# Optimization experiments

Hardware: AMD Instinct MI355X
Metric: run time of the kernel (lower is better)

Reference implementation:

```python
import jax, jax.numpy as jnp
import numpy as np

K = 16          # knn neighbors (init kwarg k)
GROUPS = 4      # GroupNorm groups
EPS = 1e-5
SLOPE = 0.2     # LeakyReLU negative slope


def fps(xyz, n):
    """Farthest point sampling. xyz: (B,N,3) -> idx (B,n). First index is 0 (pointnet2 convention)."""
    B, N, _ = xyz.shape

    def step(carry, _):
        dist, last = carry
        p = jnp.take_along_axis(xyz, last[:, None, None], axis=1)  # (B,1,3)
        d = jnp.sum((xyz - p) ** 2, axis=-1)                       # (B,N)
        dist = jnp.minimum(dist, d)
        nxt = jnp.argmax(dist, axis=-1).astype(jnp.int32)
        return (dist, nxt), nxt

    init = (jnp.full((B, N), jnp.inf, xyz.dtype), jnp.zeros((B,), jnp.int32))
    _, idxs = jax.lax.scan(step, init, None, length=n - 1)  # (n-1, B)
    return jnp.concatenate([jnp.zeros((B, 1), jnp.int32), idxs.T], axis=1)


def graph_feature(cq, fq, ck, fk):
    """DGCNN edge features. cq:(B,Q,3) fq:(B,Q,C) ck:(B,N,3) fk:(B,N,C) -> (B,Q,K,2C)."""
    d2 = (jnp.sum(cq * cq, -1)[:, :, None]
          - 2.0 * jnp.einsum('bqc,bnc->bqn', cq, ck)
          + jnp.sum(ck * ck, -1)[:, None, :])        # (B,Q,N)
    _, idx = jax.lax.top_k(-d2, K)                    # (B,Q,K) nearest first
    nb = jax.vmap(lambda f_, i_: f_[i_])(fk, idx)     # (B,Q,K,C)
    ctr = jnp.broadcast_to(fq[:, :, None, :], nb.shape)
    return jnp.concatenate([nb - ctr, ctr], axis=-1)


def conv_gn_lrelu(y, W, gw, gb):
    """1x1 Conv2d (no bias) + GroupNorm(4) + LeakyReLU(0.2). y: (B,Q,K,Cin), W: (Cout,Cin)."""
    y = jnp.einsum('bqkc,oc->bqko', y, W)
    B, Q, Kk, C = y.shape
    yg = y.reshape(B, Q * Kk, GROUPS, C // GROUPS)
    m = yg.mean(axis=(1, 3), keepdims=True)
    v = yg.var(axis=(1, 3), keepdims=True)
    y = ((yg - m) * jax.lax.rsqrt(v + EPS)).reshape(B, Q, Kk, C) * gw + gb
    return jnp.where(y > 0, y, SLOPE * y)


def setup_inputs() -> dict:
    key = jax.random.key(0)
    ks = jax.random.split(key, 16)
    B, N = 8, 4096
    s = lambda k_, shape, scale=0.1: (jax.random.normal(k_, shape, jnp.float32) * scale)
    return {
        'x': jax.random.normal(ks[0], (B, N, 7), jnp.float32),
        'W_in': s(ks[1], (8, 3), 0.5), 'b_in': s(ks[2], (8,), 0.02),
        'W1': s(ks[3], (32, 16), 0.2), 'g1w': jnp.ones((32,), jnp.float32), 'g1b': jnp.zeros((32,), jnp.float32),
        'W2': s(ks[4], (64, 64), 0.1), 'g2w': jnp.ones((64,), jnp.float32), 'g2b': jnp.zeros((64,), jnp.float32),
        'W3': s(ks[5], (64, 128), 0.1), 'g3w': jnp.ones((64,), jnp.float32), 'g3b': jnp.zeros((64,), jnp.float32),
        'W4': s(ks[6], (128, 128), 0.1), 'g4w': jnp.ones((128,), jnp.float32), 'g4b': jnp.zeros((128,), jnp.float32),
        'num0': 1024,
    }


def reference(x, W_in, b_in, W1, g1w, g1b, W2, g2w, g2b, W3, g3w, g3b, W4, g4w, g4b, num0):
    coor, normal, plane = x[..., :3], x[..., 3:6], x[..., 6:7]   # (B,N,3),(B,N,3),(B,N,1)

    # input_trans: Conv1d(3,8,1)
    f = jnp.einsum('bnc,oc->bno', coor, W_in) + b_in             # (B,N,8)

    g = graph_feature(coor, f, coor, f)                          # (B,N,K,16)
    f = conv_gn_lrelu(g, W1, g1w, g1b).max(axis=2)               # (B,N,32)

    idx = fps(coor, num0)
    gather = lambda a: jnp.take_along_axis(a, idx[:, :, None], axis=1)
    coor_q, normal_q, plane_q, f_q = gather(coor), gather(normal), gather(plane), gather(f)

    g = graph_feature(coor_q, f_q, coor, f)                      # (B,num0,K,64)
    f = conv_gn_lrelu(g, W2, g2w, g2b).max(axis=2)               # (B,num0,64)
    coor, normal, plane = coor_q, normal_q, plane_q

    g = graph_feature(coor, f, coor, f)                          # (B,num0,K,128)
    f = conv_gn_lrelu(g, W3, g3w, g3b).max(axis=2)               # (B,num0,64)

    idx = fps(coor, num0)  # source uses num[0] again
    gather = lambda a: jnp.take_along_axis(a, idx[:, :, None], axis=1)
    coor_q, normal_q, plane_q, f_q = gather(coor), gather(normal), gather(plane), gather(f)

    g = graph_feature(coor_q, f_q, coor, f)                      # (B,num0,K,128)
    f = conv_gn_lrelu(g, W4, g4w, g4b).max(axis=2)               # (B,num0,128)

    return coor_q, f, normal_q, plane_q
```

## Files before the change

kernel.cpp:

```cpp
#include <hip/hip_runtime.h>
#include <cstdint>

static constexpr int B   = 8;
static constexpr int N0  = 4096;
static constexpr int NQ  = 1024;
static constexpr int KNB = 16;

__device__ __forceinline__ unsigned long long wave_max_u64_l63(unsigned long long k) {
#define STEPU_(ctrl)                                                                    \
  {                                                                                     \
    unsigned lo_ = (unsigned)k, hi_ = (unsigned)(k >> 32);                              \
    unsigned plo_ = (unsigned)__builtin_amdgcn_update_dpp((int)lo_, (int)lo_, ctrl,     \
                                                          0xf, 0xf, false);             \
    unsigned phi_ = (unsigned)__builtin_amdgcn_update_dpp((int)hi_, (int)hi_, ctrl,     \
                                                          0xf, 0xf, false);             \
    unsigned long long pk_ = ((unsigned long long)phi_ << 32) | plo_;                   \
    if (pk_ > k) k = pk_;                                                               \
  }
  STEPU_(0x111) STEPU_(0x112) STEPU_(0x114) STEPU_(0x118) STEPU_(0x142) STEPU_(0x143)
#undef STEPU_
  return k;
}

__device__ __forceinline__ float gnf(float mx, float mn, float scv, float mo, float gb) {
  float sel = (scv >= 0.f) ? mx : mn;
  float v = (sel - mo) * scv + gb;
  return (v > 0.f) ? v : 0.2f * v;
}

__global__ void prep_kernel(const float* __restrict__ x,
                            const float* __restrict__ W_in,
                            const float* __restrict__ b_in,
                            const float* __restrict__ W1,
                            float4* __restrict__ c4, float* __restrict__ nrm,
                            float* __restrict__ pl, float* __restrict__ f0,
                            float* __restrict__ ctrY1) {
  int i = blockIdx.x * 256 + threadIdx.x;
  if (i >= B * N0) return;
  const float* xp = x + (size_t)i * 7;
  float cx = xp[0], cy = xp[1], cz = xp[2];
  float kk = __fadd_rn(__fadd_rn(__fmul_rn(cx, cx), __fmul_rn(cy, cy)), __fmul_rn(cz, cz));
  c4[i] = make_float4(cx, cy, cz, kk);
  nrm[i * 3 + 0] = xp[3]; nrm[i * 3 + 1] = xp[4]; nrm[i * 3 + 2] = xp[5];
  pl[i] = xp[6];
  float f[8];
#pragma unroll
  for (int o = 0; o < 8; o++) {
    f[o] = cx * W_in[o * 3 + 0] + cy * W_in[o * 3 + 1] + cz * W_in[o * 3 + 2] + b_in[o];
    f0[(size_t)i * 8 + o] = f[o];
  }
#pragma unroll
  for (int o = 0; o < 32; o++) {
    const float* wp = W1 + (size_t)o * 16 + 8;
    float acc = 0.f;
#pragma unroll
    for (int c = 0; c < 8; c++) acc = fmaf(f[c], wp[c], acc);
    ctrY1[(size_t)i * 32 + o] = acc;
  }
}

template <int NC>
__device__ __forceinline__ void knn_body(int bq, int lane,
                                         const float4* __restrict__ q4,
                                         const float4* __restrict__ k4,
                                         int Q, int Nk, int* __restrict__ out) {
  int b = bq / Q;
  float4 q = q4[bq];
  const float4* kb = k4 + (size_t)b * Nk + lane;
  const float INF    = __int_as_float(0x7f800000);
  const float NEGINF = __int_as_float(0xff800000);
  float myd = INF;
  int   myi = 0;
  float kth = INF;
  const bool isl0 = (lane & 15) == 0;
  constexpr int G = (NC >= 8) ? 8 : NC;
  for (int c0 = 0; c0 < NC; c0 += G) {
    float dg[G];
#pragma unroll
    for (int u = 0; u < G; u++) {
      float4 kp = kb[(c0 + u) * 64];
      float dot = __fadd_rn(__fadd_rn(__fmul_rn(q.x, kp.x), __fmul_rn(q.y, kp.y)),
                            __fmul_rn(q.z, kp.z));
      dg[u] = __fadd_rn(__fsub_rn(q.w, __fmul_rn(2.0f, dot)), kp.w);
    }
#pragma unroll
    for (int u = 0; u < G; u++) {
      float d = dg[u];
      unsigned long long msk = __ballot(d < kth);
      while (msk) {
        int j = __builtin_ctzll(msk);
        float dv = __int_as_float(__builtin_amdgcn_readlane(__float_as_int(d), j));
        int   iv = (c0 + u) * 64 + j;
        bool gt = (myd > dv);
        float pd = __int_as_float(__builtin_amdgcn_update_dpp(
            0, __float_as_int(myd), 0x111, 0xf, 0xf, true));
        int   pi = __builtin_amdgcn_update_dpp(0, myi, 0x111, 0xf, 0xf, true);
        pd = isl0 ? NEGINF : pd;
        bool tp = (pd > dv);
        float nd = tp ? pd : dv;
        int   ni = tp ? pi : iv;
        myd = gt ? nd : myd;
        myi = gt ? ni : myi;
        kth = __int_as_float(__builtin_amdgcn_readlane(__float_as_int(myd), 15));
        msk = __ballot(d < kth);
        msk = (j < 63) ? (msk & (~0ull << (j + 1))) : 0ull;
      }
    }
  }
  if (lane < KNB) out[(size_t)bq * KNB + lane] = myi;
}

template <int NPTS>
__device__ __forceinline__ void fps_body(const float4* __restrict__ cb, int* w) {
  constexpr int BLK = 256;
  constexpr int M = NPTS / BLK;
  constexpr int NW = BLK / 64;
  __shared__ __align__(16) float2 sxy[NPTS];
  __shared__ float szz[NPTS];
  __shared__ __align__(16) unsigned long long skey[2][NW];
  const int tid = threadIdx.x;
  const int wid = tid >> 6, lane = tid & 63;
  float cx[M], cy[M], cz[M], dist[M];
#pragma unroll
  for (int i = 0; i < M; i++) {
    float4 p = cb[tid * M + i];
    cx[i] = p.x; cy[i] = p.y; cz[i] = p.z;
    dist[i] = 3.4e38f;
    sxy[tid * M + i] = make_float2(p.x, p.y);
    szz[tid * M + i] = p.z;
  }
  w[0] = w[1] = w[2] = w[3] = 0;
  float4 p0 = cb[0];
  float px = p0.x, py = p0.y, pz = p0.z;
  __syncthreads();
  for (int t = 1; t < NQ; t++) {
    float bv = -1.f; int bi = 0;
#pragma unroll
    for (int i = 0; i < M; i++) {
      float dx = __fsub_rn(cx[i], px), dy = __fsub_rn(cy[i], py), dz = __fsub_rn(cz[i], pz);
      float d = __fadd_rn(__fadd_rn(__fmul_rn(dx, dx), __fmul_rn(dy, dy)), __fmul_rn(dz, dz));
      float dd = dist[i]; dd = (d < dd) ? d : dd; dist[i] = dd;
      if (dd > bv) { bv = dd; bi = tid * M + i; }
    }
    unsigned long long k =
        ((unsigned long long)__float_as_uint(bv) << 12) | (unsigned)(4095 - bi);
    k = wave_max_u64_l63(k);
    int p = t & 1;
    if (lane == 63) skey[p][wid] = k;
    __syncthreads();
    ulonglong2 ab = *(const ulonglong2*)&skey[p][0];
    ulonglong2 cd = *(const ulonglong2*)&skey[p][2];
    unsigned long long m0 = (ab.x > ab.y) ? ab.x : ab.y;
    unsigned long long m1 = (cd.x > cd.y) ? cd.x : cd.y;
    unsigned long long mk = (m0 > m1) ? m0 : m1;
    int win = 4095 - (int)(mk & 0xFFFull);
    float2 pxy = sxy[win];
    px = pxy.x; py = pxy.y; pz = szz[win];
    if (t == tid) w[0] = win;
    if (t == tid + 256) w[1] = win;
    if (t == tid + 512) w[2] = win;
    if (t == tid + 768) w[3] = win;
  }
}

template <int NC, int CF, int CO>
__device__ __forceinline__ void knnec_body(
    int blkid, const float4* __restrict__ q4, const float4* __restrict__ k4,
    const float* __restrict__ fq, const float* __restrict__ fk,
    const float* __restrict__ Wfull, const float* __restrict__ ctrY,
    const int* __restrict__ ridx,
    float* __restrict__ ymin, float* __restrict__ ymax,
    float* __restrict__ gstats, int Q, int Nk) {
  constexpr int J = CO / 4;
  constexpr int SEC = J * CF + 8;
  __shared__ float Wl[4 * SEC];
  __shared__ float sstat[8];
  for (int t = threadIdx.x; t < CO * CF; t += 256) {
    int o = t / CF, c = t % CF;
    Wl[(o / J) * SEC + (o % J) * CF + c] = Wfull[(size_t)o * (2 * CF) + c];
  }
  if (threadIdx.x < 8) sstat[threadIdx.x] = 0.0f;
  __syncthreads();
  const int wid = threadIdx.x >> 6, lane = threadIdx.x & 63;
  const int bq = blkid * 4 + wid;
  const int b = bq / Q;
  float4 q = q4[bq];
  const float4* kb = k4 + (size_t)b * Nk + lane;
  const float INF    = __int_as_float(0x7f800000);
  const float NEGINF = __int_as_float(0xff800000);
  float myd = INF;
  int   myi = 0;
  float kth = INF;
  const bool isl0 = (lane & 15) == 0;
  constexpr int G = (NC >= 8) ? 8 : NC;
  for (int c0 = 0; c0 < NC; c0 += G) {
    float dg[G];
#pragma unroll
    for (int u = 0; u < G; u++) {
      float4 kp = kb[(c0 + u) * 64];
      float dot = __fadd_rn(__fadd_rn(__fmul_rn(q.x, kp.x), __fmul_rn(q.y, kp.y)),
                            __fmul_rn(q.z, kp.z));
      dg[u] = __fadd_rn(__fsub_rn(q.w, __fmul_rn(2.0f, dot)), kp.w);
    }
#pragma unroll
    for (int u = 0; u < G; u++) {
      float d = dg[u];
      unsigned long long msk = __ballot(d < kth);
      while (msk) {
        int j = __builtin_ctzll(msk);
        float dv = __int_as_float(__builtin_amdgcn_readlane(__float_as_int(d), j));
        int   iv = (c0 + u) * 64 + j;
        bool gt = (myd > dv);
        float pd = __int_as_float(__builtin_amdgcn_update_dpp(
            0, __float_as_int(myd), 0x111, 0xf, 0xf, true));
        int   pi = __builtin_amdgcn_update_dpp(0, myi, 0x111, 0xf, 0xf, true);
        pd = isl0 ? NEGINF : pd;
        bool tp = (pd > dv);
        float nd = tp ? pd : dv;
        int   nI = tp ? pi : iv;
        myd = gt ? nd : myd;
        myi = gt ? nI : myi;
        kth = __int_as_float(__builtin_amdgcn_readlane(__float_as_int(myd), 15));
        msk = __ballot(d < kth);
        msk = (j < 63) ? (msk & (~0ull << (j + 1))) : 0ull;
      }
    }
  }
  const int g = lane >> 4;
  const int ni = myi;
  const float* nbp = fk + (size_t)(b * Nk + ni) * CF;
  const float* cp = ridx ? fq + ((size_t)b * Nk + ridx[bq]) * CF
                         : fq + (size_t)bq * CF;
  float acc[J];
#pragma unroll
  for (int j = 0; j < J; j++) acc[j] = 0.0f;
  const float* wg = &Wl[g * SEC];
#pragma unroll
  for (int c = 0; c < CF; c += 4) {
    float4 nb4 = *(const float4*)(nbp + c);
    float4 c4  = *(const float4*)(cp + c);
    float e0 = nb4.x - c4.x, e1 = nb4.y - c4.y, e2 = nb4.z - c4.z, e3 = nb4.w - c4.w;
#pragma unroll
    for (int j = 0; j < J; j++) {
      float4 w4 = *(const float4*)(wg + j * CF + c);
      acc[j] = fmaf(e0, w4.x, acc[j]);
      acc[j] = fmaf(e1, w4.y, acc[j]);
      acc[j] = fmaf(e2, w4.z, acc[j]);
      acc[j] = fmaf(e3, w4.w, acc[j]);
    }
  }
  float s = 0.f, s2 = 0.f;
  const float* cyp = ctrY + (size_t)bq * CO + g * J;
#pragma unroll
  for (int j = 0; j < J; j++) {
    float y = acc[j] + cyp[j];
    acc[j] = y;
    s += y; s2 = fmaf(y, y, s2);
  }
  float mn[J];
#pragma unroll
  for (int j = 0; j < J; j++) mn[j] = acc[j];
#pragma unroll
  for (int m = 1; m < 16; m <<= 1) {
#pragma unroll
    for (int j = 0; j < J; j++) {
      float a = __shfl_xor(acc[j], m); if (a > acc[j]) acc[j] = a;
      float c2 = __shfl_xor(mn[j], m); if (c2 < mn[j]) mn[j] = c2;
    }
    s  += __shfl_xor(s, m);
    s2 += __shfl_xor(s2, m);
  }
  if ((lane & 15) == 0) {
    float* mnp = ymin + (size_t)bq * CO + g * J;
    float* mxp = ymax + (size_t)bq * CO + g * J;
#pragma unroll
    for (int j = 0; j < J; j++) { mnp[j] = mn[j]; mxp[j] = acc[j]; }
    atomicAdd(&sstat[g], s);
    atomicAdd(&sstat[4 + g], s2);
  }
  __syncthreads();
  if (threadIdx.x < 8) atomicAdd(&gstats[b * 8 + threadIdx.x], sstat[threadIdx.x]);
}

template <int NC, int CF, int CO, bool HAS_KNN>
__device__ __forceinline__ void ec_gn_core(
    int blkid, const float4* __restrict__ q4, const float4* __restrict__ k4,
    const int* __restrict__ knn,
    const float* __restrict__ yminP, const float* __restrict__ ymaxP,
    const float* __restrict__ gstP, const float* __restrict__ gwP,
    const float* __restrict__ gbP, float invP,
    const float* __restrict__ Wfull, const int* __restrict__ ridx,
    float* __restrict__ ymin, float* __restrict__ ymax,
    float* __restrict__ gstats, int Q, int Nk) {
  constexpr int J = CO / 4;
  constexpr int SEC = J * CF + 8;
  __shared__ float Wl[4 * SEC];
  __shared__ float sstat[8];
  __shared__ __align__(16) float t_scv[CF];
  __shared__ __align__(16) float t_mo[CF];
  __shared__ __align__(16) float t_gb[CF];
  __shared__ __align__(16) float wfc[4][CF];
  __shared__ float scy[4][CO];
  const int b = (blkid * 4) / Q;
  for (int t = threadIdx.x; t < CO * CF; t += 256) {
    int o = t / CF, c = t % CF;
    Wl[(o / J) * SEC + (o % J) * CF + c] = Wfull[(size_t)o * (2 * CF) + c];
  }
  if (threadIdx.x < CF) {
    int c = threadIdx.x;
    int gg = c / (CF / 4);
    float m  = gstP[b * 8 + gg] * invP;
    float s2 = gstP[b * 8 + 4 + gg] * invP;
    float rs = rsqrtf(s2 - m * m + 1e-5f);
    t_scv[c] = gwP[c] * rs;
    t_mo[c]  = m;
    t_gb[c]  = gbP[c];
  }
  if (threadIdx.x < 8) sstat[threadIdx.x] = 0.0f;
  __syncthreads();
  const int wid = threadIdx.x >> 6, lane = threadIdx.x & 63;
  const int bq = blkid * 4 + wid;
  size_t cbase = (ridx ? ((size_t)b * Nk + ridx[bq]) : (size_t)bq) * CF;
  if (lane < CF)
    wfc[wid][lane] = gnf(ymaxP[cbase + lane], yminP[cbase + lane],
                         t_scv[lane], t_mo[lane], t_gb[lane]);
  for (int oo = lane; oo < CO; oo += 64) {
    const float* wp = Wfull + (size_t)oo * (2 * CF) + CF;
    float acc0 = 0.f;
#pragma unroll
    for (int c = 0; c < CF; c++) acc0 = fmaf(wfc[wid][c], wp[c], acc0);
    scy[wid][oo] = acc0;
  }
  int ni;
  if (HAS_KNN) {
    float4 q = q4[bq];
    const float4* kb = k4 + (size_t)b * Nk + lane;
    const float INF    = __int_as_float(0x7f800000);
    const float NEGINF = __int_as_float(0xff800000);
    float myd = INF;
    int   myi = 0;
    float kth = INF;
    const bool isl0 = (lane & 15) == 0;
    constexpr int G = (NC >= 8) ? 8 : NC;
    for (int c0 = 0; c0 < NC; c0 += G) {
      float dg[G];
#pragma unroll
      for (int u = 0; u < G; u++) {
        float4 kp = kb[(c0 + u) * 64];
        float dot = __fadd_rn(__fadd_rn(__fmul_rn(q.x, kp.x), __fmul_rn(q.y, kp.y)),
                              __fmul_rn(q.z, kp.z));
        dg[u] = __fadd_rn(__fsub_rn(q.w, __fmul_rn(2.0f, dot)), kp.w);
      }
#pragma unroll
      for (int u = 0; u < G; u++) {
        float d = dg[u];
        unsigned long long msk = __ballot(d < kth);
        while (msk) {
          int j = __builtin_ctzll(msk);
          float dv = __int_as_float(__builtin_amdgcn_readlane(__float_as_int(d), j));
          int   iv = (c0 + u) * 64 + j;
          bool gt = (myd > dv);
          float pd = __int_as_float(__builtin_amdgcn_update_dpp(
              0, __float_as_int(myd), 0x111, 0xf, 0xf, true));
          int   pi = __builtin_amdgcn_update_dpp(0, myi, 0x111, 0xf, 0xf, true);
          pd = isl0 ? NEGINF : pd;
          bool tp = (pd > dv);
          float nd = tp ? pd : dv;
          int   nI = tp ? pi : iv;
          myd = gt ? nd : myd;
          myi = gt ? nI : myi;
          kth = __int_as_float(__builtin_amdgcn_readlane(__float_as_int(myd), 15));
          msk = __ballot(d < kth);
          msk = (j < 63) ? (msk & (~0ull << (j + 1))) : 0ull;
        }
      }
    }
    ni = myi;
  } else {
    ni = knn[(size_t)bq * KNB + (lane & 15)];
  }
  const int g = lane >> 4;
  size_t nbase = ((size_t)b * Nk + ni) * CF;
  float acc[J];
#pragma unroll
  for (int j = 0; j < J; j++) acc[j] = 0.0f;
  const float* wg = &Wl[g * SEC];
#pragma unroll
  for (int c = 0; c < CF; c += 4) {
    float4 mx4 = *(const float4*)(ymaxP + nbase + c);
    float4 mn4 = *(const float4*)(yminP + nbase + c);
    float4 sc4 = *(const float4*)(&t_scv[c]);
    float4 mo4 = *(const float4*)(&t_mo[c]);
    float4 gb4 = *(const float4*)(&t_gb[c]);
    float4 c4  = *(const float4*)(&wfc[wid][c]);
    float e0 = gnf(mx4.x, mn4.x, sc4.x, mo4.x, gb4.x) - c4.x;
    float e1 = gnf(mx4.y, mn4.y, sc4.y, mo4.y, gb4.y) - c4.y;
    float e2 = gnf(mx4.z, mn4.z, sc4.z, mo4.z, gb4.z) - c4.z;
    float e3 = gnf(mx4.w, mn4.w, sc4.w, mo4.w, gb4.w) - c4.w;
#pragma unroll
    for (int j = 0; j < J; j++) {
      float4 w4 = *(const float4*)(wg + j * CF + c);
      acc[j] = fmaf(e0, w4.x, acc[j]);
      acc[j] = fmaf(e1, w4.y, acc[j]);
      acc[j] = fmaf(e2, w4.z, acc[j]);
      acc[j] = fmaf(e3, w4.w, acc[j]);
    }
  }
  float s = 0.f, s2 = 0.f;
#pragma unroll
  for (int j = 0; j < J; j++) {
    float y = acc[j] + scy[wid][g * J + j];
    acc[j] = y;
    s += y; s2 = fmaf(y, y, s2);
  }
  float mn[J];
#pragma unroll
  for (int j = 0; j < J; j++) mn[j] = acc[j];
#pragma unroll
  for (int m = 1; m < 16; m <<= 1) {
#pragma unroll
    for (int j = 0; j < J; j++) {
      float a = __shfl_xor(acc[j], m); if (a > acc[j]) acc[j] = a;
      float c2 = __shfl_xor(mn[j], m); if (c2 < mn[j]) mn[j] = c2;
    }
    s  += __shfl_xor(s, m);
    s2 += __shfl_xor(s2, m);
  }
  if ((lane & 15) == 0) {
    float* mnp = ymin + (size_t)bq * CO + g * J;
    float* mxp = ymax + (size_t)bq * CO + g * J;
#pragma unroll
    for (int j = 0; j < J; j++) { mnp[j] = mn[j]; mxp[j] = acc[j]; }
    atomicAdd(&sstat[g], s);
    atomicAdd(&sstat[4 + g], s2);
  }
  __syncthreads();
  if (threadIdx.x < 8) atomicAdd(&gstats[b * 8 + threadIdx.x], sstat[threadIdx.x]);
}

__global__ __launch_bounds__(256, 2) void mega1_kernel(
    const float4* __restrict__ c40, const float* __restrict__ nrm,
    const float* __restrict__ pl, const float* __restrict__ f0,
    const float* __restrict__ W1, const float* __restrict__ ctrY1,
    int* __restrict__ idx1,
    float4* __restrict__ c4q1, float* __restrict__ nq1, float* __restrict__ pq1,
    float* __restrict__ ymin, float* __restrict__ ymax, float* __restrict__ gst1) {
  int blk = blockIdx.x;
  if (blk < 8) {
    const int b = blk, tid = threadIdx.x;
    const float4* cb = c40 + (size_t)b * N0;
    int w[4];
    fps_body<N0>(cb, w);
    int* idxb = idx1 + (size_t)b * NQ;
#pragma unroll
    for (int u = 0; u < 4; u++) {
      int r = tid + u * 256;
      int s = (u == 0 && tid == 0) ? 0 : w[u];
      idxb[r] = s;
      c4q1[(size_t)b * NQ + r] = cb[s];
      const float* np = nrm + ((size_t)b * N0 + s) * 3;
      float* ndp = nq1 + ((size_t)b * NQ + r) * 3;
      ndp[0] = np[0]; ndp[1] = np[1]; ndp[2] = np[2];
      pq1[(size_t)b * NQ + r] = pl[(size_t)b * N0 + s];
    }
  } else {
    knnec_body<64, 8, 32>(blk - 8, c40, c40, f0, f0, W1, ctrY1, nullptr,
                          ymin, ymax, gst1, N0, N0);
  }
}

__global__ __launch_bounds__(256, 2) void mega2_kernel(
    const float4* __restrict__ c40, const float4* __restrict__ c4q1,
    const float* __restrict__ nq1, const float* __restrict__ pq1,
    const float* __restrict__ yminA, const float* __restrict__ ymaxA,
    const float* __restrict__ gst1, const float* __restrict__ g1w,
    const float* __restrict__ g1b, float inv1,
    const int* __restrict__ idx1, const float* __restrict__ W2,
    float* __restrict__ yminB, float* __restrict__ ymaxB, float* __restrict__ gst2,
    int* __restrict__ idx2, float4* __restrict__ c4q2,
    float* __restrict__ cq2out, float* __restrict__ nq2out,
    float* __restrict__ pq2out, int* __restrict__ knnB) {
  int blk = blockIdx.x;
  if (blk < 8) {
    const int b = blk, tid = threadIdx.x;
    const float4* cqb = c4q1 + (size_t)b * NQ;
    int w[4];
    fps_body<NQ>(cqb, w);
    int* idxb = idx2 + (size_t)b * NQ;
#pragma unroll
    for (int u = 0; u < 4; u++) {
      int r = tid + u * 256;
      int s = (u == 0 && tid == 0) ? 0 : w[u];
      idxb[r] = s;
      float4 c = cqb[s];
      c4q2[(size_t)b * NQ + r] = c;
      float* cd = cq2out + ((size_t)b * NQ + r) * 3;
      cd[0] = c.x; cd[1] = c.y; cd[2] = c.z;
      const float* np = nq1 + ((size_t)b * NQ + s) * 3;
      float* ndp = nq2out + ((size_t)b * NQ + r) * 3;
      ndp[0] = np[0]; ndp[1] = np[1]; ndp[2] = np[2];
      pq2out[(size_t)b * NQ + r] = pq1[(size_t)b * NQ + s];
    }
  } else if (blk < 8 + 2048) {
    ec_gn_core<64, 32, 64, true>(blk - 8, c4q1, c40, nullptr,
                                 yminA, ymaxA, gst1, g1w, g1b, inv1,
                                 W2, idx1, yminB, ymaxB, gst2, NQ, N0);
  } else {
    int bq = (blk - (8 + 2048)) * 4 + (threadIdx.x >> 6);
    knn_body<16>(bq, threadIdx.x & 63, c4q1, c4q1, NQ, NQ, knnB);
  }
}

__global__ __launch_bounds__(256) void ec3g_kernel(
    const int* __restrict__ knnB,
    const float* __restrict__ yminB, const float* __restrict__ ymaxB,
    const float* __restrict__ gst2, const float* __restrict__ g2w,
    const float* __restrict__ g2b, float inv2,
    const float* __restrict__ W3,
    float* __restrict__ yminC, float* __restrict__ ymaxC, float* __restrict__ gst3) {
  ec_gn_core<16, 64, 64, false>(blockIdx.x, nullptr, nullptr, knnB,
                                yminB, ymaxB, gst2, g2w, g2b, inv2,
                                W3, nullptr, yminC, ymaxC, gst3, NQ, NQ);
}

__global__ __launch_bounds__(256) void mega3g_kernel(
    const float4* __restrict__ c4q1, const float4* __restrict__ c4q2,
    const float* __restrict__ yminC, const float* __restrict__ ymaxC,
    const float* __restrict__ gst3, const float* __restrict__ g3w,
    const float* __restrict__ g3b, float inv3,
    const int* __restrict__ idx2, const float* __restrict__ W4,
    float* __restrict__ yminD, float* __restrict__ ymaxD, float* __restrict__ gst4) {
  ec_gn_core<16, 64, 128, true>(blockIdx.x, c4q2, c4q1, nullptr,
                                yminC, ymaxC, gst3, g3w, g3b, inv3,
                                W4, idx2, yminD, ymaxD, gst4, NQ, NQ);
}

template <int CO>
__global__ void gn_out_kernel(const float* __restrict__ ymin, const float* __restrict__ ymax,
                              const float* __restrict__ gstats, const float* __restrict__ gw,
                              const float* __restrict__ gb, float* __restrict__ fout,
                              int total, int Q, float inv_cnt) {
  int i = blockIdx.x * 256 + threadIdx.x;
  if (i >= total) return;
  constexpr int J = CO / 4;
  int o = i % CO; int bq = i / CO; int b = bq / Q;
  int g = o / J;
  float m  = gstats[b * 8 + g] * inv_cnt;
  float s2 = gstats[b * 8 + 4 + g] * inv_cnt;
  float rs = rsqrtf(s2 - m * m + 1e-5f);
  float sc = gw[o] * rs;
  float sel = (sc >= 0.f) ? ymax[i] : ymin[i];
  float v = (sel - m) * sc + gb[o];
  fout[i] = (v > 0.f) ? v : 0.2f * v;
}

extern "C" void kernel_launch(void* const* d_in, const int* in_sizes, int n_in,
                              void* d_out, int out_size, void* d_ws, size_t ws_size,
                              hipStream_t stream) {
  (void)in_sizes; (void)n_in; (void)out_size; (void)ws_size;
  const float* x    = (const float*)d_in[0];
  const float* W_in = (const float*)d_in[1];
  const float* b_in = (const float*)d_in[2];
  const float* W1   = (const float*)d_in[3];
  const float* g1w  = (const float*)d_in[4];
  const float* g1b  = (const float*)d_in[5];
  const float* W2   = (const float*)d_in[6];
  const float* g2w  = (const float*)d_in[7];
  const float* g2b  = (const float*)d_in[8];
  const float* W3   = (const float*)d_in[9];
  const float* g3w  = (const float*)d_in[10];
  const float* g3b  = (const float*)d_in[11];
  const float* W4   = (const float*)d_in[12];
  const float* g4w  = (const float*)d_in[13];
  const float* g4b  = (const float*)d_in[14];

  float* ws = (float*)d_ws;
  size_t o_c40   = 0;
  size_t o_nrm   = o_c40   + (size_t)B * N0 * 4;
  size_t o_pl    = o_nrm   + (size_t)B * N0 * 3;
  size_t o_f0    = o_pl    + (size_t)B * N0;
  size_t o_ctrY1 = o_f0    + (size_t)B * N0 * 8;
  size_t o_yAmin = o_ctrY1 + (size_t)B * N0 * 32;
  size_t o_yAmax = o_yAmin + (size_t)B * N0 * 32;
  size_t o_yBmin = o_yAmax + (size_t)B * N0 * 32;
  size_t o_yBmax = o_yBmin + (size_t)B * NQ * 64;
  size_t o_yCmin = o_yBmax + (size_t)B * NQ * 64;
  size_t o_yCmax = o_yCmin + (size_t)B * NQ * 64;
  size_t o_knnB  = o_yCmax + (size_t)B * NQ * 64;
  size_t o_gst   = o_knnB  + (size_t)B * NQ * KNB;
  size_t o_idx1  = o_gst   + 4 * B * 8;
  size_t o_idx2  = o_idx1  + (size_t)B * NQ;
  size_t o_c4q1  = o_idx2  + (size_t)B * NQ;
  size_t o_c4q2  = o_c4q1  + (size_t)B * NQ * 4;
  size_t o_nq1   = o_c4q2  + (size_t)B * NQ * 4;
  size_t o_pq1   = o_nq1   + (size_t)B * NQ * 3;

  float4* c40   = (float4*)(ws + o_c40);
  float*  nrm   = ws + o_nrm;    float* pl    = ws + o_pl;
  float*  f0    = ws + o_f0;     float* ctrY1 = ws + o_ctrY1;
  float*  yAmin = ws + o_yAmin;  float* yAmax = ws + o_yAmax;
  float*  yBmin = ws + o_yBmin;  float* yBmax = ws + o_yBmax;
  float*  yCmin = ws + o_yCmin;  float* yCmax = ws + o_yCmax;
  float*  yDmin = ctrY1;
  float*  yDmax = yAmin;
  int*    knnB  = (int*)(ws + o_knnB);
  float*  gst   = ws + o_gst;
  int*    idx1  = (int*)(ws + o_idx1);
  int*    idx2  = (int*)(ws + o_idx2);
  float4* c4q1  = (float4*)(ws + o_c4q1);
  float4* c4q2  = (float4*)(ws + o_c4q2);
  float*  nq1   = ws + o_nq1;    float* pq1   = ws + o_pq1;

  float* out  = (float*)d_out;
  float* cq2  = out;
  float* fout = out + (size_t)B * NQ * 3;
  float* nq2  = fout + (size_t)B * NQ * 128;
  float* pq2  = nq2 + (size_t)B * NQ * 3;

  const float inv1 = 1.0f / (4096.0f * 16.0f * 8.0f);
  const float inv2 = 1.0f / (1024.0f * 16.0f * 16.0f);
  const float inv3 = 1.0f / (1024.0f * 16.0f * 16.0f);
  const float inv4 = 1.0f / (1024.0f * 16.0f * 32.0f);

  hipMemsetAsync(gst, 0, 4 * B * 8 * sizeof(float), stream);

  prep_kernel<<<(B * N0 + 255) / 256, 256, 0, stream>>>(x, W_in, b_in, W1,
                                                        c40, nrm, pl, f0, ctrY1);

  mega1_kernel<<<8 + 8192, 256, 0, stream>>>(c40, nrm, pl, f0, W1, ctrY1,
                                             idx1, c4q1, nq1, pq1,
                                             yAmin, yAmax, gst + 0);

  mega2_kernel<<<8 + 2048 + 2048, 256, 0, stream>>>(
      c40, c4q1, nq1, pq1, yAmin, yAmax, gst + 0, g1w, g1b, inv1,
      idx1, W2, yBmin, yBmax, gst + B * 8,
      idx2, c4q2, cq2, nq2, pq2, knnB);

  ec3g_kernel<<<B * NQ / 4, 256, 0, stream>>>(
      knnB, yBmin, yBmax, gst + B * 8, g2w, g2b, inv2, W3,
      yCmin, yCmax, gst + 2 * B * 8);

  mega3g_kernel<<<B * NQ / 4, 256, 0, stream>>>(
      c4q1, c4q2, yCmin, yCmax, gst + 2 * B * 8, g3w, g3b, inv3,
      idx2, W4, yDmin, yDmax, gst + 3 * B * 8);

  gn_out_kernel<128><<<(B * NQ * 128 + 255) / 256, 256, 0, stream>>>(
      yDmin, yDmax, gst + 3 * B * 8, g4w, g4b, fout, B * NQ * 128, NQ, inv4);
}
```

Baseline: 1.438 ms.

## Run second-stage FPS in a single wavefront with barrier-free DPP reductions

Replaces the 256-thread farthest-point-sampling loop over the 1024 sampled points with a single-wavefront version. Each lane keeps 16 points in registers, and the argmax uses DPP shuffles plus ballot/readlane instead of LDS exchanges and a __syncthreads per iteration. This targets the per-step barrier and cross-wave latency on the serial FPS chain in mega2. Launch bounds are relaxed from 2 to 1 blocks per CU, which may raise register use and lower occupancy for the edge-conv and kNN blocks that share the kernel.

```diff
diff --git a/kernel.cpp b/kernel.cpp
--- a/kernel.cpp
+++ b/kernel.cpp
@@ -160,6 +160,50 @@
     if (t == tid + 256) w[1] = win;
     if (t == tid + 512) w[2] = win;
     if (t == tid + 768) w[3] = win;
+  }
+}
+
+template <int NPTS>
+__device__ __forceinline__ void fps1w_body(const float4* __restrict__ cb,
+                                           int* __restrict__ swin) {
+  constexpr int M = NPTS / 64;
+  const int lane = threadIdx.x;
+  float cx[M], cy[M], cz[M], dist[M];
+#pragma unroll
+  for (int i = 0; i < M; i++) {
+    float4 p = cb[lane * M + i];
+    cx[i] = p.x; cy[i] = p.y; cz[i] = p.z;
+    dist[i] = 3.4e38f;
+  }
+  float4 p0 = cb[0];
+  float px = p0.x, py = p0.y, pz = p0.z;
+  for (int t = 1; t < NQ; t++) {
+    float bv = -1.f; int bi = 0;
+    float bx = px, by = py, bz = pz;
+#pragma unroll
+    for (int i = 0; i < M; i++) {
+      float dx = __fsub_rn(cx[i], px), dy = __fsub_rn(cy[i], py), dz = __fsub_rn(cz[i], pz);
+      float d = __fadd_rn(__fadd_rn(__fmul_rn(dx, dx), __fmul_rn(dy, dy)), __fmul_rn(dz, dz));
+      float dd = dist[i]; dd = (d < dd) ? d : dd; dist[i] = dd;
+      if (dd > bv) { bv = dd; bi = lane * M + i; bx = cx[i]; by = cy[i]; bz = cz[i]; }
+    }
+    float wm = bv;
+#define SMAX_(ctrl)                                                                     \
+  {                                                                                     \
+    int t_ = __builtin_amdgcn_update_dpp(__float_as_int(wm), __float_as_int(wm), ctrl,  \
+                                         0xf, 0xf, false);                              \
+    wm = fmaxf(wm, __int_as_float(t_));                                                 \
+  }
+    SMAX_(0x111) SMAX_(0x112) SMAX_(0x114) SMAX_(0x118) SMAX_(0x142) SMAX_(0x143)
+#undef SMAX_
+    float wmax = __int_as_float(__builtin_amdgcn_readlane(__float_as_int(wm), 63));
+    unsigned long long tied = __ballot(bv == wmax);
+    int L = (int)__builtin_ctzll(tied);
+    int win = __builtin_amdgcn_readlane(bi, L);
+    px = __int_as_float(__builtin_amdgcn_readlane(__float_as_int(bx), L));
+    py = __int_as_float(__builtin_amdgcn_readlane(__float_as_int(by), L));
+    pz = __int_as_float(__builtin_amdgcn_readlane(__float_as_int(bz), L));
+    if (lane == 0) swin[t] = win;
   }
 }
 
@@ -469,7 +513,7 @@
   }
 }
 
-__global__ __launch_bounds__(256, 2) void mega2_kernel(
+__global__ __launch_bounds__(256, 1) void mega2_kernel(
     const float4* __restrict__ c40, const float4* __restrict__ c4q1,
     const float* __restrict__ nq1, const float* __restrict__ pq1,
     const float* __restrict__ yminA, const float* __restrict__ ymaxA,
@@ -482,24 +526,26 @@
     float* __restrict__ pq2out, int* __restrict__ knnB) {
   int blk = blockIdx.x;
   if (blk < 8) {
-    const int b = blk, tid = threadIdx.x;
-    const float4* cqb = c4q1 + (size_t)b * NQ;
-    int w[4];
-    fps_body<NQ>(cqb, w);
-    int* idxb = idx2 + (size_t)b * NQ;
-#pragma unroll
-    for (int u = 0; u < 4; u++) {
-      int r = tid + u * 256;
-      int s = (u == 0 && tid == 0) ? 0 : w[u];
-      idxb[r] = s;
-      float4 c = cqb[s];
-      c4q2[(size_t)b * NQ + r] = c;
-      float* cd = cq2out + ((size_t)b * NQ + r) * 3;
-      cd[0] = c.x; cd[1] = c.y; cd[2] = c.z;
-      const float* np = nq1 + ((size_t)b * NQ + s) * 3;
-      float* ndp = nq2out + ((size_t)b * NQ + r) * 3;
-      ndp[0] = np[0]; ndp[1] = np[1]; ndp[2] = np[2];
-      pq2out[(size_t)b * NQ + r] = pq1[(size_t)b * NQ + s];
+    if (threadIdx.x < 64) {
+      __shared__ int swin2[NQ];
+      const int b = blk, lane = threadIdx.x;
+      const float4* cqb = c4q1 + (size_t)b * NQ;
+      fps1w_body<NQ>(cqb, swin2);
+      int* idxb = idx2 + (size_t)b * NQ;
+#pragma unroll
+      for (int u = 0; u < NQ / 64; u++) {
+        int r = lane + u * 64;
+        int s = (r == 0) ? 0 : swin2[r];
+        idxb[r] = s;
+        float4 c = cqb[s];
+        c4q2[(size_t)b * NQ + r] = c;
+        float* cd = cq2out + ((size_t)b * NQ + r) * 3;
+        cd[0] = c.x; cd[1] = c.y; cd[2] = c.z;
+        const float* np = nq1 + ((size_t)b * NQ + s) * 3;
+        float* ndp = nq2out + ((size_t)b * NQ + r) * 3;
+        ndp[0] = np[0]; ndp[1] = np[1]; ndp[2] = np[2];
+        pq2out[(size_t)b * NQ + r] = pq1[(size_t)b * NQ + s];
+      }
     }
   } else if (blk < 8 + 2048) {
     ec_gn_core<64, 32, 64, true>(blk - 8, c4q1, c40, nullptr,
```

Result: slower. 1.857 ms (+29.1%).
